# Kernel tuning notes

Measured on AMD Instinct MI355X. Metric: run time of the kernel, lower is better.

The kernel has to match this reference:

```python
import jax, jax.numpy as jnp
import numpy as np

N_E, FEAT, REST = 2048, 512, 8
HEAD, LENGTH = 8, 64


def setup_inputs() -> dict:
    key = jax.random.key(0)
    kx, kq, kk, kd = jax.random.split(key, 4)
    x = jax.random.normal(kx, (N_E, FEAT, REST), dtype=jnp.float32)
    Q = jax.random.normal(kq, (HEAD, LENGTH, FEAT), dtype=jnp.float32)
    K = jax.random.normal(kk, (HEAD, LENGTH, FEAT), dtype=jnp.float32)
    D = jax.random.normal(kd, (HEAD, LENGTH, FEAT), dtype=jnp.float32)
    return {"x": x, "Q": Q, "K": K, "D": D}


def _linear(a, W):
    # a: (n, f, *rest), W: (h, q, f) -> y: (n, h, q, *rest)
    y = jnp.einsum('nf...,hqf->nhq...', a, W)
    # L2-normalize over the last 3 axes (here: h? no -- axes (q, rest...) per the
    # original code: sum over (-1,-2,-3) of (n,h,q,rest) = (h,q,rest) per n)
    norm = jnp.sqrt((y * y).sum((-1, -2, -3), keepdims=True))
    return y / norm


def reference(x, Q, K, D):
    n_e = x.shape[0]
    rest = x.shape[2:]
    head, length = Q.shape[0], Q.shape[1]
    q = _linear(x, Q)  # (n, h, l, rest)
    k = _linear(x, K)
    d = _linear(x, D)
    # scores over electrons: contract (l, rest) -> (h, n, n)
    w = jax.nn.softmax(jnp.einsum('nh...,mh...->hnm', q, k), axis=-1)
    # weighted combine: (h,n,m) x (m,h,l,rest) -> (n,h,l,rest)
    v = jnp.einsum('hnm,mhl...->nhl...', w, d)
    return v.reshape((n_e, head * length) + rest)
```

## Files before the change

### kernel.cpp

```cpp
#include <hip/hip_runtime.h>
#include <math.h>

#define NE   2048
#define FEAT 512

typedef short short8 __attribute__((ext_vector_type(8)));
typedef float f32x4  __attribute__((ext_vector_type(4)));

__device__ __forceinline__ unsigned short f2bf(float f) {
    union { float f; unsigned u; } v; v.f = f;
    unsigned r = v.u + 0x7fffu + ((v.u >> 16) & 1u);
    return (unsigned short)(r >> 16);
}
__device__ __forceinline__ float bf2f(unsigned b) {
    union { unsigned u; float f; } v; v.u = b << 16;
    return v.f;
}
__device__ __forceinline__ unsigned pack2(float a, float b) {
    return (unsigned)f2bf(a) | ((unsigned)f2bf(b) << 16);
}

__device__ __forceinline__ void gld16(unsigned short* lds, const unsigned short* g) {
    __builtin_amdgcn_global_load_lds(
        (const __attribute__((address_space(1))) unsigned int*)g,
        (__attribute__((address_space(3))) unsigned int*)lds,
        16, 0, 0);
}

__device__ __forceinline__ void bar() {
    asm volatile("" ::: "memory");
    __builtin_amdgcn_s_barrier();
    asm volatile("" ::: "memory");
}
#define VMW(n) asm volatile("s_waitcnt vmcnt(" #n ")" ::: "memory")


__global__ __launch_bounds__(256) void wconv_kernel(
    const float* __restrict__ Wq, const float* __restrict__ Wk, const float* __restrict__ Wd,
    unsigned short* __restrict__ wbf)
{
    const int t = threadIdx.x;
    const float* W = (blockIdx.y == 0) ? Wq : (blockIdx.y == 1) ? Wk : Wd;
    unsigned short* o = wbf + (size_t)blockIdx.y * 262144;
    const int idx = blockIdx.x * 2048 + t * 8;
    const float4* p = (const float4*)(W + idx);
    float4 v0 = p[0], v1 = p[1];
    *(uint4*)(o + idx) = make_uint4(pack2(v0.x, v0.y), pack2(v0.z, v0.w),
                                    pack2(v1.x, v1.y), pack2(v1.z, v1.w));
}

__global__ __launch_bounds__(256) void xpose_kernel(const float* __restrict__ x,
                                                    unsigned short* __restrict__ xt)
{
    __shared__ float xs[8 * 516];
    const int t = threadIdx.x;
    const int n = blockIdx.x;
    const float4* xp = (const float4*)(x + (size_t)n * 4096);
    #pragma unroll
    for (int i = 0; i < 4; ++i) {
        int idx = t + 256 * i;
        float4 v = xp[idx];
        int f = idx >> 1, rh = (idx & 1) * 4;
        xs[(rh + 0) * 516 + f] = v.x;
        xs[(rh + 1) * 516 + f] = v.y;
        xs[(rh + 2) * 516 + f] = v.z;
        xs[(rh + 3) * 516 + f] = v.w;
    }
    __syncthreads();
    const int r = t >> 5, f0 = (t & 31) * 16;
    const float* src = &xs[r * 516 + f0];
    unsigned o[8];
    #pragma unroll
    for (int j = 0; j < 8; ++j) o[j] = pack2(src[2 * j], src[2 * j + 1]);
    unsigned short* dst = xt + (size_t)n * 4096 + r * 512 + f0;
    *(uint4*)dst       = make_uint4(o[0], o[1], o[2], o[3]);
    *(uint4*)(dst + 8) = make_uint4(o[4], o[5], o[6], o[7]);
}

__global__ __launch_bounds__(256) void proj_gemm(
    const unsigned short* __restrict__ wbf, const unsigned short* __restrict__ xt,
    unsigned short* __restrict__ qb, unsigned short* __restrict__ kb, unsigned short* __restrict__ db)
{
    __shared__ unsigned short SM[17408];
    const int t = threadIdx.x;
    const int w = blockIdx.z;
    const unsigned short* W = wbf + (size_t)w * 262144;
    unsigned short* out = (w == 0) ? qb : (w == 1) ? kb : db;
    const int M0 = blockIdx.y * 128;
    const int N0 = blockIdx.x * 128;
    const int wave = t >> 6, lane = t & 63, quad = lane >> 4, l16 = lane & 15;
    const int lrow = lane >> 3;
    const int scol = ((lane & 7) ^ lrow) * 8;
    unsigned short* As = SM;
    unsigned short* Bs = SM + 8192;

    f32x4 acc[2][8];
    #pragma unroll
    for (int i = 0; i < 2; ++i)
        #pragma unroll
        for (int j = 0; j < 8; ++j) acc[i][j] = {0.f, 0.f, 0.f, 0.f};

    for (int kc = 0; kc < 8; ++kc) {
        #pragma unroll
        for (int p = 0; p < 4; ++p) {
            int c = p * 4 + wave;
            gld16(As + c * 512, W  + (size_t)(M0 + c * 8 + lrow) * 512 + kc * 64 + scol);
            gld16(Bs + c * 512, xt + (size_t)(N0 + c * 8 + lrow) * 512 + kc * 64 + scol);
        }
        __syncthreads();
        #pragma unroll
        for (int kk = 0; kk < 2; ++kk) {
            int so = ((kk * 4 + quad) ^ (l16 & 7)) * 8;
            short8 a0 = *(const short8*)&As[(wave * 32 + l16) * 64 + so];
            short8 a1 = *(const short8*)&As[(wave * 32 + 16 + l16) * 64 + so];
            #pragma unroll
            for (int ct = 0; ct < 8; ++ct) {
                short8 bb = *(const short8*)&Bs[(ct * 16 + l16) * 64 + so];
                acc[0][ct] = __builtin_amdgcn_mfma_f32_16x16x32_bf16(a0, bb, acc[0][ct], 0, 0, 0);
                acc[1][ct] = __builtin_amdgcn_mfma_f32_16x16x32_bf16(a1, bb, acc[1][ct], 0, 0, 0);
            }
        }
        __syncthreads();
    }

    unsigned short* T = SM;
    #pragma unroll
    for (int rt = 0; rt < 2; ++rt)
        #pragma unroll
        for (int reg = 0; reg < 4; ++reg) {
            int row = wave * 32 + rt * 16 + quad * 4 + reg;
            #pragma unroll
            for (int ct = 0; ct < 8; ++ct)
                T[row * 136 + ct * 16 + l16] = f2bf(acc[rt][ct][reg]);
        }
    __syncthreads();
    #pragma unroll
    for (int i = 0; i < 8; ++i) {
        int c = t + 256 * i;
        int n = c >> 7, row = c & 127;
        uint4 v = *(const uint4*)(T + row * 136 + n * 8);
        int hl = M0 + row;
        unsigned short* dst = out + (size_t)(hl >> 6) * 1048576 + (size_t)(hl & 63) * 8
                                  + (size_t)((N0 >> 3) + n) * 512;
        *(uint4*)dst = v;
    }
}

__global__ __launch_bounds__(256) void scales_kernel(
    const unsigned short* __restrict__ qb, const unsigned short* __restrict__ kb,
    const unsigned short* __restrict__ db, float* __restrict__ scales)
{
    __shared__ float red[256];
    const int t = threadIdx.x;
    const int n = blockIdx.x, w = blockIdx.y;
    const unsigned short* src = (w == 0) ? qb : (w == 1) ? kb : db;
    const int h = t >> 5, f0 = (t & 31) * 16;
    const unsigned short* p = src + ((size_t)h * NE + n) * 512 + f0;
    uint4 v0 = *(const uint4*)p;
    uint4 v1 = *(const uint4*)(p + 8);
    unsigned a[8] = {v0.x, v0.y, v0.z, v0.w, v1.x, v1.y, v1.z, v1.w};
    float s = 0.f;
    #pragma unroll
    for (int j = 0; j < 8; ++j) {
        float lo = bf2f(a[j] & 0xffffu), hi = bf2f(a[j] >> 16);
        s += lo * lo + hi * hi;
    }
    red[t] = s;
    __syncthreads();
    for (int st = 128; st > 0; st >>= 1) {
        if (t < st) red[t] += red[t + st];
        __syncthreads();
    }
    if (t == 0) scales[w * NE + n] = rsqrtf(red[0]);
}

__global__ __launch_bounds__(256) void dtrans_kernel(
    const unsigned short* __restrict__ db, const float* __restrict__ invd,
    unsigned short* __restrict__ dT)
{
    __shared__ float Ts[64 * 68];
    const int t = threadIdx.x;
    const int h = blockIdx.z, n0 = blockIdx.y * 64, f0 = blockIdx.x * 64;
    const int rr = t >> 3, cs = (t & 7) * 8;
    #pragma unroll
    for (int p = 0; p < 2; ++p) {
        int row = rr + p * 32;
        float sc = invd[n0 + row];
        uint4 v = *(const uint4*)(db + ((size_t)h * NE + n0 + row) * 512 + f0 + cs);
        unsigned a[4] = {v.x, v.y, v.z, v.w};
        float* d = &Ts[row * 68 + cs];
        #pragma unroll
        for (int j = 0; j < 4; ++j) {
            d[2 * j]     = bf2f(a[j] & 0xffffu) * sc;
            d[2 * j + 1] = bf2f(a[j] >> 16) * sc;
        }
    }
    __syncthreads();
    const int f = t >> 2, ns = (t & 3) * 16;
    unsigned o[8];
    #pragma unroll
    for (int j = 0; j < 8; ++j)
        o[j] = pack2(Ts[(ns + 2 * j) * 68 + f], Ts[(ns + 2 * j + 1) * 68 + f]);
    unsigned short* dst = dT + ((size_t)h * 512 + f0 + f) * NE + n0 + ns;
    *(uint4*)dst       = make_uint4(o[0], o[1], o[2], o[3]);
    *(uint4*)(dst + 8) = make_uint4(o[4], o[5], o[6], o[7]);
}

__global__ __launch_bounds__(512, 2) void score_kernel(
    const unsigned short* __restrict__ qb, const unsigned short* __restrict__ kb,
    const float* __restrict__ scales, unsigned short* __restrict__ P,
    float* __restrict__ sums, int g)
{
    __shared__ unsigned short SM[65536];
    const int t = threadIdx.x;
    int bid = blockIdx.x + 8 * (blockIdx.y + 8 * blockIdx.z);
    int swz = (bid & 7) * 32 + (bid >> 3);
    const int bx = swz & 7, by = (swz >> 3) & 7, bz = swz >> 6;
    const int hg = bz, h = g * 4 + hg;
    const int n0 = by * 256, m0 = bx * 256;
    const int wave = t >> 6, lane = t & 63, quad = lane >> 4, l16 = lane & 15;
    const int wr = wave >> 2, wc = wave & 3;
    const int lrow = lane >> 3;
    const int scol = ((lane & 7) ^ lrow) * 8;
    const unsigned short* qh = qb + (size_t)h * NE * 512;
    const unsigned short* kh = kb + (size_t)h * NE * 512;

    f32x4 acc[8][4];
    #pragma unroll
    for (int m = 0; m < 8; ++m)
        #pragma unroll
        for (int n = 0; n < 4; ++n) acc[m][n] = {0.f, 0.f, 0.f, 0.f};

    auto STAGE = [&](int kc, int buf) {
        unsigned short* A = SM + buf * 16384;
        unsigned short* B = SM + 32768 + buf * 16384;
        #pragma unroll
        for (int p = 0; p < 4; ++p) {
            int c = p * 8 + wave;
            gld16(A + c * 512, qh + (size_t)(n0 + c * 8 + lrow) * 512 + kc * 64 + scol);
        }
        #pragma unroll
        for (int p = 0; p < 4; ++p) {
            int c = p * 8 + wave;
            gld16(B + c * 512, kh + (size_t)(m0 + c * 8 + lrow) * 512 + kc * 64 + scol);
        }
    };
    auto COMPUTE = [&](int buf) {
        const unsigned short* A = SM + buf * 16384;
        const unsigned short* B = SM + 32768 + buf * 16384;
        #pragma unroll
        for (int kk = 0; kk < 2; ++kk) {
            int so = ((kk * 4 + quad) ^ (l16 & 7)) * 8;
            short8 a[8], b[4];
            #pragma unroll
            for (int m = 0; m < 8; ++m)
                a[m] = *(const short8*)&A[(wr * 128 + m * 16 + l16) * 64 + so];
            #pragma unroll
            for (int n = 0; n < 4; ++n)
                b[n] = *(const short8*)&B[(wc * 64 + n * 16 + l16) * 64 + so];
            #pragma unroll
            for (int m = 0; m < 8; ++m)
                #pragma unroll
                for (int n = 0; n < 4; ++n)
                    acc[m][n] = __builtin_amdgcn_mfma_f32_16x16x32_bf16(a[m], b[n], acc[m][n], 0, 0, 0);
        }
    };

    STAGE(0, 0);
    STAGE(1, 1);
    for (int kc = 0; kc < 8; ++kc) {
        if (kc < 7) { VMW(8); } else { VMW(0); }
        bar();
        COMPUTE(kc & 1);
        bar();
        if (kc + 2 < 8) STAGE(kc + 2, kc & 1);
    }

    float ik[4];
    #pragma unroll
    for (int n = 0; n < 4; ++n) ik[n] = scales[NE + m0 + wc * 64 + n * 16 + l16];

    unsigned short* Ph = P + (size_t)hg * NE * NE;
    #pragma unroll
    for (int m = 0; m < 8; ++m)
        #pragma unroll
        for (int reg = 0; reg < 4; ++reg) {
            int row = n0 + wr * 128 + m * 16 + quad * 4 + reg;
            float qs = scales[row];
            unsigned short* prow = Ph + (size_t)row * NE + m0 + wc * 64;
            float rs = 0.f;
            #pragma unroll
            for (int n = 0; n < 4; ++n) {
                float e = __expf(acc[m][n][reg] * qs * ik[n]);
                unsigned short bx16 = f2bf(e);
                prow[n * 16 + l16] = bx16;
                rs += bf2f(bx16);
            }
            rs += __shfl_xor(rs, 1);
            rs += __shfl_xor(rs, 2);
            rs += __shfl_xor(rs, 4);
            rs += __shfl_xor(rs, 8);
            if (l16 == 0) atomicAdd(&sums[hg * NE + row], rs);
        }
}

__global__ __launch_bounds__(512) void combine_kernel(
    const unsigned short* __restrict__ P, const unsigned short* __restrict__ dT,
    const float* __restrict__ sums, float* __restrict__ out, int g)
{
    __shared__ unsigned short Ps[2][8192];
    __shared__ unsigned short Ds[2][8192];
    const int t = threadIdx.x;
    int bid = blockIdx.x + 4 * (blockIdx.y + 16 * blockIdx.z);
    int swz = (bid & 7) * 32 + (bid >> 3);
    const int bx = swz & 3, by = (swz >> 2) & 15, bz = swz >> 6;
    const int hg = bz, h = g * 4 + hg;
    const int n0 = by * 128, f0 = bx * 128;
    const int wave = t >> 6, lane = t & 63, quad = lane >> 4, l16 = lane & 15;
    const int wn = wave >> 1, wf = wave & 1;
    const int lrow = lane >> 3;
    const int scol = ((lane & 7) ^ lrow) * 8;
    const unsigned short* Ph = P + (size_t)hg * NE * NE;
    const unsigned short* dh = dT + (size_t)h * 512 * NE;

    f32x4 acc[2][4];
    #pragma unroll
    for (int i = 0; i < 2; ++i)
        #pragma unroll
        for (int j = 0; j < 4; ++j) acc[i][j] = {0.f, 0.f, 0.f, 0.f};

    auto STAGE = [&](int mc, int buf) {
        #pragma unroll
        for (int p = 0; p < 2; ++p) {
            int c = p * 8 + wave;
            gld16(&Ps[buf][c * 512], Ph + (size_t)(n0 + c * 8 + lrow) * NE + mc * 64 + scol);
            gld16(&Ds[buf][c * 512], dh + (size_t)(f0 + c * 8 + lrow) * NE + mc * 64 + scol);
        }
    };
    auto COMPUTE = [&](int buf) {
        #pragma unroll
        for (int kk = 0; kk < 2; ++kk) {
            int so = ((kk * 4 + quad) ^ (l16 & 7)) * 8;
            short8 a0 = *(const short8*)&Ps[buf][(wn * 32 + l16) * 64 + so];
            short8 a1 = *(const short8*)&Ps[buf][(wn * 32 + 16 + l16) * 64 + so];
            #pragma unroll
            for (int ct = 0; ct < 4; ++ct) {
                short8 bb = *(const short8*)&Ds[buf][(wf * 64 + ct * 16 + l16) * 64 + so];
                acc[0][ct] = __builtin_amdgcn_mfma_f32_16x16x32_bf16(a0, bb, acc[0][ct], 0, 0, 0);
                acc[1][ct] = __builtin_amdgcn_mfma_f32_16x16x32_bf16(a1, bb, acc[1][ct], 0, 0, 0);
            }
        }
    };

    STAGE(0, 0);
    STAGE(1, 1);
    for (int mc = 0; mc < 32; ++mc) {
        if (mc < 31) { VMW(4); } else { VMW(0); }
        bar();
        COMPUTE(mc & 1);
        bar();
        if (mc + 2 < 32) STAGE(mc + 2, mc & 1);
    }

    #pragma unroll
    for (int rt = 0; rt < 2; ++rt)
        #pragma unroll
        for (int reg = 0; reg < 4; ++reg) {
            int nl = wn * 32 + rt * 16 + quad * 4 + reg;
            float li = 1.0f / sums[hg * NE + n0 + nl];
            float* orow = out + (size_t)(n0 + nl) * 4096 + h * 512 + f0 + wf * 64;
            #pragma unroll
            for (int ct = 0; ct < 4; ++ct)
                orow[ct * 16 + l16] = acc[rt][ct][reg] * li;
        }
}

extern "C" void kernel_launch(void* const* d_in, const int* in_sizes, int n_in,
                              void* d_out, int out_size, void* d_ws, size_t ws_size,
                              hipStream_t stream)
{
    const float* x  = (const float*)d_in[0];
    const float* Qw = (const float*)d_in[1];
    const float* Kw = (const float*)d_in[2];
    const float* Dw = (const float*)d_in[3];
    float* out = (float*)d_out;

    char* ws = (char*)d_ws;
    unsigned short* xt = (unsigned short*)ws;
    unsigned short* db = (unsigned short*)(ws + 16777216);
    unsigned short* P  = (unsigned short*)ws;
    unsigned short* qb = (unsigned short*)(ws + 33554432);
    unsigned short* kb = (unsigned short*)(ws + 33554432 + 16777216);
    unsigned short* dT = (unsigned short*)(ws + 33554432 + 2 * 16777216);
    unsigned short* wbf = dT;
    float* scales = (float*)(ws + 83886080);
    float* sums   = (float*)(ws + 83886080 + 24576);

    wconv_kernel<<<dim3(128, 3), 256, 0, stream>>>(Qw, Kw, Dw, wbf);
    xpose_kernel<<<2048, 256, 0, stream>>>(x, xt);
    proj_gemm<<<dim3(128, 4, 3), 256, 0, stream>>>(wbf, xt, qb, kb, db);
    scales_kernel<<<dim3(2048, 3), 256, 0, stream>>>(qb, kb, db, scales);
    dtrans_kernel<<<dim3(8, 32, 8), 256, 0, stream>>>(db, scales + 2 * NE, dT);
    for (int g = 0; g < 2; ++g) {
        hipMemsetAsync(sums, 0, 4 * NE * sizeof(float), stream);
        score_kernel<<<dim3(8, 8, 4), 512, 0, stream>>>(qb, kb, scales, P, sums, g);
        combine_kernel<<<dim3(4, 16, 4), 512, 0, stream>>>(P, dT, sums, out, g);
    }
}
```

Baseline: 268.5 us.

## Fuse norm reduction into projection GEMM, enlarge tiles, single-buffer combine

The projection GEMM now uses 512-thread blocks with 256x128 tiles, a swizzled block order and double-buffered async LDS staging. Its epilogue computes per-electron sums of squares from the fp32 accumulators and atomically adds them into a buffer, so the separate scales kernel that re-read q/k/d is replaced by a tiny rsqrt kernel. The combine kernel goes back to single-buffered staging with plain __syncthreads, which halves its LDS use but no longer overlaps loads with compute. Norms now come from fp32 accumulators rather than bf16-rounded values, and atomics make the summation order nondeterministic.

```diff
diff --git a/kernel.cpp b/kernel.cpp
--- a/kernel.cpp
+++ b/kernel.cpp
@@ -77,101 +77,130 @@
     *(uint4*)(dst + 8) = make_uint4(o[4], o[5], o[6], o[7]);
 }
 
-__global__ __launch_bounds__(256) void proj_gemm(
+__global__ __launch_bounds__(512, 1) void proj_gemm(
     const unsigned short* __restrict__ wbf, const unsigned short* __restrict__ xt,
-    unsigned short* __restrict__ qb, unsigned short* __restrict__ kb, unsigned short* __restrict__ db)
-{
-    __shared__ unsigned short SM[17408];
-    const int t = threadIdx.x;
-    const int w = blockIdx.z;
+    unsigned short* __restrict__ qb, unsigned short* __restrict__ kb, unsigned short* __restrict__ db,
+    float* __restrict__ s2)
+{
+    __shared__ unsigned short SM[49152];
+    const int t = threadIdx.x;
+    int bid = blockIdx.x + 128 * (blockIdx.y + 2 * blockIdx.z);
+    int swz = (bid & 7) * 96 + (bid >> 3);
+    const int bx = swz & 127, rest = swz >> 7;
+    const int my = rest & 1, w = rest >> 1;
     const unsigned short* W = wbf + (size_t)w * 262144;
     unsigned short* out = (w == 0) ? qb : (w == 1) ? kb : db;
-    const int M0 = blockIdx.y * 128;
-    const int N0 = blockIdx.x * 128;
+    const int M0 = my * 256;
+    const int N0 = bx * 128;
     const int wave = t >> 6, lane = t & 63, quad = lane >> 4, l16 = lane & 15;
+    const int wr = wave >> 1, wc = wave & 1;
     const int lrow = lane >> 3;
     const int scol = ((lane & 7) ^ lrow) * 8;
-    unsigned short* As = SM;
-    unsigned short* Bs = SM + 8192;
-
-    f32x4 acc[2][8];
-    #pragma unroll
-    for (int i = 0; i < 2; ++i)
-        #pragma unroll
-        for (int j = 0; j < 8; ++j) acc[i][j] = {0.f, 0.f, 0.f, 0.f};
-
-    for (int kc = 0; kc < 8; ++kc) {
+
+    f32x4 acc[4][4];
+    #pragma unroll
+    for (int m = 0; m < 4; ++m)
+        #pragma unroll
+        for (int n = 0; n < 4; ++n) acc[m][n] = {0.f, 0.f, 0.f, 0.f};
+
+    auto STAGE = [&](int kc, int buf) {
+        unsigned short* A = SM + buf * 16384;
+        unsigned short* B = SM + 32768 + buf * 8192;
         #pragma unroll
         for (int p = 0; p < 4; ++p) {
-            int c = p * 4 + wave;
-            gld16(As + c * 512, W  + (size_t)(M0 + c * 8 + lrow) * 512 + kc * 64 + scol);
-            gld16(Bs + c * 512, xt + (size_t)(N0 + c * 8 + lrow) * 512 + kc * 64 + scol);
-        }
-        __syncthreads();
+            int c = p * 8 + wave;
+            gld16(A + c * 512, W + (size_t)(M0 + c * 8 + lrow) * 512 + kc * 64 + scol);
+        }
+        #pragma unroll
+        for (int p = 0; p < 2; ++p) {
+            int c = p * 8 + wave;
+            gld16(B + c * 512, xt + (size_t)(N0 + c * 8 + lrow) * 512 + kc * 64 + scol);
+        }
+    };
+    auto COMPUTE = [&](int buf) {
+        const unsigned short* A = SM + buf * 16384;
+        const unsigned short* B = SM + 32768 + buf * 8192;
         #pragma unroll
         for (int kk = 0; kk < 2; ++kk) {
             int so = ((kk * 4 + quad) ^ (l16 & 7)) * 8;
-            short8 a0 = *(const short8*)&As[(wave * 32 + l16) * 64 + so];
-            short8 a1 = *(const short8*)&As[(wave * 32 + 16 + l16) * 64 + so];
-            #pragma unroll
-            for (int ct = 0; ct < 8; ++ct) {
-                short8 bb = *(const short8*)&Bs[(ct * 16 + l16) * 64 + so];
-                acc[0][ct] = __builtin_amdgcn_mfma_f32_16x16x32_bf16(a0, bb, acc[0][ct], 0, 0, 0);
-                acc[1][ct] = __builtin_amdgcn_mfma_f32_16x16x32_bf16(a1, bb, acc[1][ct], 0, 0, 0);
-            }
-        }
-        __syncthreads();
+            short8 a[4], b[4];
+            #pragma unroll
+            for (int m = 0; m < 4; ++m)
+                a[m] = *(const short8*)&A[(wr * 64 + m * 16 + l16) * 64 + so];
+            #pragma unroll
+            for (int n = 0; n < 4; ++n)
+                b[n] = *(const short8*)&B[(wc * 64 + n * 16 + l16) * 64 + so];
+            #pragma unroll
+            for (int m = 0; m < 4; ++m)
+                #pragma unroll
+                for (int n = 0; n < 4; ++n)
+                    acc[m][n] = __builtin_amdgcn_mfma_f32_16x16x32_bf16(a[m], b[n], acc[m][n], 0, 0, 0);
+        }
+    };
+
+    STAGE(0, 0);
+    STAGE(1, 1);
+    for (int kc = 0; kc < 8; ++kc) {
+        if (kc < 7) { VMW(6); } else { VMW(0); }
+        bar();
+        COMPUTE(kc & 1);
+        bar();
+        if (kc + 2 < 8) STAGE(kc + 2, kc & 1);
+    }
+
+    float cs[4];
+    #pragma unroll
+    for (int n = 0; n < 4; ++n) {
+        float s = 0.f;
+        #pragma unroll
+        for (int m = 0; m < 4; ++m)
+            #pragma unroll
+            for (int reg = 0; reg < 4; ++reg)
+                s += acc[m][n][reg] * acc[m][n][reg];
+        cs[n] = s;
+    }
+    #pragma unroll
+    for (int n = 0; n < 4; ++n) {
+        float s = cs[n];
+        s += __shfl_xor(s, 16);
+        s += __shfl_xor(s, 32);
+        s += __shfl_xor(s, 1);
+        s += __shfl_xor(s, 2);
+        s += __shfl_xor(s, 4);
+        if ((lane & 7) == 0 && lane < 16) {
+            int n_elec = (N0 >> 3) + wc * 8 + n * 2 + (lane >> 3);
+            atomicAdd(&s2[w * NE + n_elec], s);
+        }
     }
 
     unsigned short* T = SM;
     #pragma unroll
-    for (int rt = 0; rt < 2; ++rt)
+    for (int m = 0; m < 4; ++m)
         #pragma unroll
         for (int reg = 0; reg < 4; ++reg) {
-            int row = wave * 32 + rt * 16 + quad * 4 + reg;
-            #pragma unroll
-            for (int ct = 0; ct < 8; ++ct)
-                T[row * 136 + ct * 16 + l16] = f2bf(acc[rt][ct][reg]);
+            int row = wr * 64 + m * 16 + quad * 4 + reg;
+            #pragma unroll
+            for (int n = 0; n < 4; ++n)
+                T[row * 136 + wc * 64 + n * 16 + l16] = f2bf(acc[m][n][reg]);
         }
     __syncthreads();
     #pragma unroll
     for (int i = 0; i < 8; ++i) {
-        int c = t + 256 * i;
-        int n = c >> 7, row = c & 127;
-        uint4 v = *(const uint4*)(T + row * 136 + n * 8);
+        int c = t + 512 * i;
+        int row = c & 255, cb = c >> 8;
+        uint4 v = *(const uint4*)(T + row * 136 + cb * 8);
         int hl = M0 + row;
         unsigned short* dst = out + (size_t)(hl >> 6) * 1048576 + (size_t)(hl & 63) * 8
-                                  + (size_t)((N0 >> 3) + n) * 512;
+                                  + (size_t)((N0 >> 3) + cb) * 512;
         *(uint4*)dst = v;
     }
 }
 
-__global__ __launch_bounds__(256) void scales_kernel(
-    const unsigned short* __restrict__ qb, const unsigned short* __restrict__ kb,
-    const unsigned short* __restrict__ db, float* __restrict__ scales)
-{
-    __shared__ float red[256];
-    const int t = threadIdx.x;
-    const int n = blockIdx.x, w = blockIdx.y;
-    const unsigned short* src = (w == 0) ? qb : (w == 1) ? kb : db;
-    const int h = t >> 5, f0 = (t & 31) * 16;
-    const unsigned short* p = src + ((size_t)h * NE + n) * 512 + f0;
-    uint4 v0 = *(const uint4*)p;
-    uint4 v1 = *(const uint4*)(p + 8);
-    unsigned a[8] = {v0.x, v0.y, v0.z, v0.w, v1.x, v1.y, v1.z, v1.w};
-    float s = 0.f;
-    #pragma unroll
-    for (int j = 0; j < 8; ++j) {
-        float lo = bf2f(a[j] & 0xffffu), hi = bf2f(a[j] >> 16);
-        s += lo * lo + hi * hi;
-    }
-    red[t] = s;
-    __syncthreads();
-    for (int st = 128; st > 0; st >>= 1) {
-        if (t < st) red[t] += red[t + st];
-        __syncthreads();
-    }
-    if (t == 0) scales[w * NE + n] = rsqrtf(red[0]);
+__global__ __launch_bounds__(256) void sfinal_kernel(const float* __restrict__ s2,
+                                                     float* __restrict__ scales)
+{
+    int i = blockIdx.x * 256 + threadIdx.x;
+    scales[i] = rsqrtf(s2[i]);
 }
 
 __global__ __launch_bounds__(256) void dtrans_kernel(
@@ -308,8 +337,8 @@
     const unsigned short* __restrict__ P, const unsigned short* __restrict__ dT,
     const float* __restrict__ sums, float* __restrict__ out, int g)
 {
-    __shared__ unsigned short Ps[2][8192];
-    __shared__ unsigned short Ds[2][8192];
+    __shared__ unsigned short Ps[8192];
+    __shared__ unsigned short Ds[8192];
     const int t = threadIdx.x;
     int bid = blockIdx.x + 4 * (blockIdx.y + 16 * blockIdx.z);
     int swz = (bid & 7) * 32 + (bid >> 3);
@@ -329,37 +358,27 @@
         #pragma unroll
         for (int j = 0; j < 4; ++j) acc[i][j] = {0.f, 0.f, 0.f, 0.f};
 
-    auto STAGE = [&](int mc, int buf) {
+    for (int mc = 0; mc < 32; ++mc) {
         #pragma unroll
         for (int p = 0; p < 2; ++p) {
             int c = p * 8 + wave;
-            gld16(&Ps[buf][c * 512], Ph + (size_t)(n0 + c * 8 + lrow) * NE + mc * 64 + scol);
-            gld16(&Ds[buf][c * 512], dh + (size_t)(f0 + c * 8 + lrow) * NE + mc * 64 + scol);
-        }
-    };
-    auto COMPUTE = [&](int buf) {
+            gld16(Ps + c * 512, Ph + (size_t)(n0 + c * 8 + lrow) * NE + mc * 64 + scol);
+            gld16(Ds + c * 512, dh + (size_t)(f0 + c * 8 + lrow) * NE + mc * 64 + scol);
+        }
+        __syncthreads();
         #pragma unroll
         for (int kk = 0; kk < 2; ++kk) {
             int so = ((kk * 4 + quad) ^ (l16 & 7)) * 8;
-            short8 a0 = *(const short8*)&Ps[buf][(wn * 32 + l16) * 64 + so];
-            short8 a1 = *(const short8*)&Ps[buf][(wn * 32 + 16 + l16) * 64 + so];
+            short8 a0 = *(const short8*)&Ps[(wn * 32 + l16) * 64 + so];
+            short8 a1 = *(const short8*)&Ps[(wn * 32 + 16 + l16) * 64 + so];
             #pragma unroll
             for (int ct = 0; ct < 4; ++ct) {
-                short8 bb = *(const short8*)&Ds[buf][(wf * 64 + ct * 16 + l16) * 64 + so];
+                short8 bb = *(const short8*)&Ds[(wf * 64 + ct * 16 + l16) * 64 + so];
                 acc[0][ct] = __builtin_amdgcn_mfma_f32_16x16x32_bf16(a0, bb, acc[0][ct], 0, 0, 0);
                 acc[1][ct] = __builtin_amdgcn_mfma_f32_16x16x32_bf16(a1, bb, acc[1][ct], 0, 0, 0);
             }
         }
-    };
-
-    STAGE(0, 0);
-    STAGE(1, 1);
-    for (int mc = 0; mc < 32; ++mc) {
-        if (mc < 31) { VMW(4); } else { VMW(0); }
-        bar();
-        COMPUTE(mc & 1);
-        bar();
-        if (mc + 2 < 32) STAGE(mc + 2, mc & 1);
+        __syncthreads();
     }
 
     #pragma unroll
@@ -395,11 +414,13 @@
     unsigned short* wbf = dT;
     float* scales = (float*)(ws + 83886080);
     float* sums   = (float*)(ws + 83886080 + 24576);
+    float* s2     = (float*)(ws + 83886080 + 24576 + 32768);
 
     wconv_kernel<<<dim3(128, 3), 256, 0, stream>>>(Qw, Kw, Dw, wbf);
     xpose_kernel<<<2048, 256, 0, stream>>>(x, xt);
-    proj_gemm<<<dim3(128, 4, 3), 256, 0, stream>>>(wbf, xt, qb, kb, db);
-    scales_kernel<<<dim3(2048, 3), 256, 0, stream>>>(qb, kb, db, scales);
+    hipMemsetAsync(s2, 0, 3 * NE * sizeof(float), stream);
+    proj_gemm<<<dim3(128, 2, 3), 512, 0, stream>>>(wbf, xt, qb, kb, db, s2);
+    sfinal_kernel<<<24, 256, 0, stream>>>(s2, scales);
     dtrans_kernel<<<dim3(8, 32, 8), 256, 0, stream>>>(db, scales + 2 * NE, dT);
     for (int g = 0; g < 2; ++g) {
         hipMemsetAsync(sums, 0, 4 * NE * sizeof(float), stream);
```

Result: slower. 281.7 us (+4.9%).
